# Optimization experiments

Hardware: AMD Instinct MI355X
Metric: run time of the kernel (lower is better)

Reference implementation:

```python
import jax, jax.numpy as jnp
import numpy as np

B, N, H, E, P = 2, 20000, 128, 200000, 3


def _mlp2(x, w1, b1, w2, b2):
    # Linear -> SiLU -> Linear
    return jax.nn.silu(x @ w1 + b1) @ w2 + b2


def setup_inputs() -> dict:
    key = jax.random.key(0)
    ks = iter(jax.random.split(key, 40))
    def nrm(shape, s=0.05):
        return jax.random.normal(next(ks), shape, dtype=jnp.float32) * s
    inp = {
        "features": jax.random.normal(next(ks), (B, N, H), dtype=jnp.float32),
        "positions": jax.random.normal(next(ks), (B, N, P), dtype=jnp.float32),
        "edge_index_up": jax.random.randint(next(ks), (2, E), 0, N, dtype=jnp.int32),
        "edge_index_down": jax.random.randint(next(ks), (2, E), 0, N, dtype=jnp.int32),
        "degree_up": jax.random.uniform(next(ks), (N,), minval=1.0, maxval=32.0, dtype=jnp.float32),
        "degree_down": jax.random.uniform(next(ks), (N,), minval=1.0, maxval=32.0, dtype=jnp.float32),
    }
    for name in ("up", "down"):
        inp[f"w_msg1_{name}"] = nrm((2 * H + 1, H)); inp[f"b_msg1_{name}"] = jnp.zeros((H,), jnp.float32)
        inp[f"w_msg2_{name}"] = nrm((H, H));         inp[f"b_msg2_{name}"] = jnp.zeros((H,), jnp.float32)
        inp[f"w_pos1_{name}"] = nrm((H, H));         inp[f"b_pos1_{name}"] = jnp.zeros((H,), jnp.float32)
        inp[f"w_pos2_{name}"] = nrm((H, 1));         inp[f"b_pos2_{name}"] = jnp.zeros((1,), jnp.float32)
    inp["w_upd1"] = nrm((2 * H, H)); inp["b_upd1"] = jnp.zeros((H,), jnp.float32)
    inp["w_upd2"] = nrm((H, H));     inp["b_upd2"] = jnp.zeros((H,), jnp.float32)
    return inp


def reference(features, positions, edge_index_up, edge_index_down, degree_up, degree_down,
              w_msg1_up, b_msg1_up, w_msg2_up, b_msg2_up,
              w_pos1_up, b_pos1_up, w_pos2_up, b_pos2_up,
              w_msg1_down, b_msg1_down, w_msg2_down, b_msg2_down,
              w_pos1_down, b_pos1_down, w_pos2_down, b_pos2_down,
              w_upd1, b_upd1, w_upd2, b_upd2):
    n_neighborhoods = 2
    msg_acc = jnp.zeros_like(features)
    pos_upd = jnp.zeros_like(positions)
    neighborhoods = [
        (edge_index_up, degree_up,
         (w_msg1_up, b_msg1_up, w_msg2_up, b_msg2_up),
         (w_pos1_up, b_pos1_up, w_pos2_up, b_pos2_up)),
        (edge_index_down, degree_down,
         (w_msg1_down, b_msg1_down, w_msg2_down, b_msg2_down),
         (w_pos1_down, b_pos1_down, w_pos2_down, b_pos2_down)),
    ]
    for edge_index, degree, msg_p, pos_p in neighborhoods:
        src, dst = edge_index[0], edge_index[1]
        h_src = features[:, src, :]                     # [B, E, H] gather
        h_dst = features[:, dst, :]                     # [B, E, H] gather
        rel_pos = positions[:, src, :] - positions[:, dst, :]  # [B, E, P]
        dist = jnp.linalg.norm(rel_pos, axis=-1, keepdims=True)  # [B, E, 1]
        msg_input = jnp.concatenate([h_src, h_dst, dist], axis=-1)  # [B, E, 2H+1]
        messages = _mlp2(msg_input, *msg_p)             # [B, E, H]
        agg = jnp.zeros_like(features).at[:, dst, :].add(messages)  # scatter-add over dim 1
        agg = agg / jnp.clip(degree, 1.0, None)[None, :, None]
        msg_acc = msg_acc + agg
        weights = jnp.tanh(_mlp2(messages, *pos_p))     # [B, E, 1]
        pos_upd = pos_upd + jnp.zeros_like(positions).at[:, dst, :].add(weights * rel_pos)
    feat_update = _mlp2(jnp.concatenate([features, msg_acc], axis=-1), w_upd1, b_upd1, w_upd2, b_upd2)
    updated_features = features + feat_update
    updated_positions = positions + pos_upd / n_neighborhoods
    return updated_features, updated_positions
```

## Files before the change

### kernel.cpp

```cpp
#include <hip/hip_runtime.h>

#define BB 2
#define NN 20000
#define HH 128
#define EE 200000
#define TR 64
#define NEB 3125
#define NBLK 79
#define NWG (2 * BB * NEB)

typedef unsigned short u16;
typedef __attribute__((ext_vector_type(4))) float f32x4;
typedef __bf16 bf16x8 __attribute__((ext_vector_type(8)));

#define MFMA(a, b, c) __builtin_amdgcn_mfma_f32_16x16x32_bf16((a), (b), (c), 0, 0, 0)

__device__ __forceinline__ float bf2f(u16 u) {
    union { unsigned int i; float f; } v; v.i = ((unsigned int)u) << 16; return v.f;
}
__device__ __forceinline__ u16 f2bf(float f) {
    union { __bf16 h; u16 u; } v; v.h = (__bf16)f; return v.u;
}
#if __has_builtin(__builtin_amdgcn_rcpf)
__device__ __forceinline__ float rcpf(float x) { return __builtin_amdgcn_rcpf(x); }
#else
__device__ __forceinline__ float rcpf(float x) { return 1.f / x; }
#endif
__device__ __forceinline__ float silu_f(float z) { return z * rcpf(1.f + __expf(-z)); }
__device__ __forceinline__ float ldv(const void* p, long i, int f) {
    return f ? ((const float*)p)[i] : bf2f(((const u16*)p)[i]);
}

__global__ __launch_bounds__(256) void detect_kernel(const u16* __restrict__ f,
                                                     int* __restrict__ flag) {
    int tid = threadIdx.x;
    u16 v = f[tid * 2];
    int e = (v >> 7) & 0xFF;
    int ok = (e >= 101 && e <= 143) ? 1 : 0;
    __shared__ int c;
    if (tid == 0) c = 0;
    __syncthreads();
    atomicAdd(&c, ok);
    __syncthreads();
    if (tid == 0) *flag = (c < 200) ? 1 : 0;
}

#define C5TOT 5281540
#define FTOT 180224
#define SV 655000
#define SCT 41540
#define SB2 (SV + SCT)
#define SC2 (SB2 + FTOT)
#define SD2 (SC2 + 2 * EE)
struct P18 { const void* p[18]; };
struct P8 { const void* w[8]; };

__global__ __launch_bounds__(256) void setup_kernel(
    P18 cp, P8 wf, const int* __restrict__ eu, const int* __restrict__ ed,
    u16* __restrict__ canon, u16* __restrict__ fbase,
    int* __restrict__ cnt_up, int* __restrict__ cnt_dn, const int* __restrict__ flag)
{
    long i = (long)blockIdx.x * 256 + threadIdx.x;
    const int isf = *flag;
    if (i < SV) {
        long j = i * 8;
        if (isf) {
            const float* src = (j < 5120000)
                ? (const float*)cp.p[0] + j
                : (const float*)cp.p[1] + (j - 5120000);
            float4 v0 = *(const float4*)src;
            float4 v1 = *(const float4*)(src + 4);
            uint4 o;
            o.x = (unsigned)f2bf(v0.x) | ((unsigned)f2bf(v0.y) << 16);
            o.y = (unsigned)f2bf(v0.z) | ((unsigned)f2bf(v0.w) << 16);
            o.z = (unsigned)f2bf(v1.x) | ((unsigned)f2bf(v1.y) << 16);
            o.w = (unsigned)f2bf(v1.z) | ((unsigned)f2bf(v1.w) << 16);
            *(uint4*)&canon[j] = o;
        } else {
            const u16* src = (j < 5120000)
                ? (const u16*)cp.p[0] + j
                : (const u16*)cp.p[1] + (j - 5120000);
            *(uint4*)&canon[j] = *(const uint4*)src;
        }
        return;
    }
    long k = i - SV;
    if (k < SCT) {
        static const int off[19] = {
            0, 5120000, 5240000, 5260000, 5280000,
            5280128, 5280256, 5280384, 5280512, 5280640,
            5280642, 5280770, 5280898, 5281026, 5281154, 5281282,
            5281284, 5281412, 5281540 };
        static const int rsz[18] = {
            5120000, 120000, 20000, 20000,
            128, 128, 128, 128, 128, 1,
            128, 128, 128, 128, 128, 1,
            128, 128 };
        static const int soff[18] = {
            0, 0, 0, 0,
            32768, 0, 0, 0, 0, 0,
            32768, 0, 0, 0, 0, 0,
            0, 0 };
        int j = 5240000 + (int)k;
        int t = 0;
#pragma unroll 1
        while (j >= off[t + 1]) ++t;
        int kk = j - off[t];
        u16 v = 0;
        if (kk < rsz[t]) v = f2bf(ldv(cp.p[t], (long)soff[t] + kk, isf));
        canon[j] = v;
        return;
    }
    k -= SCT;
    if (k < FTOT) {
        static const int foff[9] = { 0, 32768, 49152, 65536, 98304, 114688,
                                     131072, 163840, 180224 };
        int j = (int)k;
        int t = 0;
#pragma unroll 1
        while (j >= foff[t + 1]) ++t;
        int m = j - foff[t];
        int jj = m & 7, lane = (m >> 3) & 63, nt = (m >> 9) & 7, kt = m >> 12;
        int kr = kt * 32 + ((lane >> 4) * 8) + jj;
        int n = nt * 16 + (lane & 15);
        fbase[j] = f2bf(ldv(wf.w[t], (long)kr * 128 + n, isf));
        return;
    }
    k -= FTOT;
    if (k < 2 * EE) {
        int e = (int)k;
        if (e < EE) atomicAdd(&cnt_up[eu[EE + e]], 1);
        else atomicAdd(&cnt_dn[ed[EE + e - EE]], 1);
    }
}

__global__ __launch_bounds__(256) void gemm_fuse_kernel(
    const void* __restrict__ w2u, const void* __restrict__ p1u,
    const void* __restrict__ b2u, const void* __restrict__ bp1u,
    const void* __restrict__ w2d, const void* __restrict__ p1d,
    const void* __restrict__ b2d, const void* __restrict__ bp1d,
    u16* __restrict__ fragu, u16* __restrict__ fragd,
    u16* __restrict__ cbp1u, u16* __restrict__ cbp1d,
    const int* __restrict__ flag)
{
    const int dir = blockIdx.x >> 6;
    const int idx = (blockIdx.x & 63) * 256 + threadIdx.x;
    const int k = idx >> 7, n = idx & 127;
    const int isf = *flag;
    const void* W2 = dir ? w2d : w2u;
    const void* P1 = dir ? p1d : p1u;
    float s = 0.f;
#pragma unroll 4
    for (int m = 0; m < 128; ++m)
        s += ldv(W2, (long)k * 128 + m, isf) * ldv(P1, (long)m * 128 + n, isf);
    u16* dst = dir ? fragd : fragu;
    dst[(((k >> 5) * 8 + (n >> 4)) * 64 + ((k >> 3) & 3) * 16 + (n & 15)) * 8 + (k & 7)] = f2bf(s);
    if (idx < 128) {
        const void* B2 = dir ? b2d : b2u;
        const void* BP1 = dir ? bp1d : bp1u;
        float t = 0.f;
#pragma unroll 4
        for (int m = 0; m < 128; ++m)
            t += ldv(B2, m, isf) * ldv(P1, (long)m * 128 + idx, isf);
        (dir ? cbp1d : cbp1u)[idx] = f2bf(t + ldv(BP1, idx, isf));
    }
}

struct SP { const int* cnt[2]; int* cur[2]; int* bsum[2]; };

__global__ __launch_bounds__(256) void scan1_kernel(SP p) {
    int half = blockIdx.x / NBLK;
    int b = blockIdx.x - half * NBLK;
    int t = threadIdx.x;
    int i = b * 256 + t;
    __shared__ int buf[256];
    int v = (i < NN) ? p.cnt[half][i] : 0;
    buf[t] = v;
    __syncthreads();
    for (int s = 1; s < 256; s <<= 1) {
        int x = (t >= s) ? buf[t - s] : 0;
        __syncthreads();
        buf[t] += x;
        __syncthreads();
    }
    if (i < NN) p.cur[half][i] = buf[t] - v;
    if (t == 255) p.bsum[half][b] = buf[255];
}

__global__ __launch_bounds__(256) void scan2_kernel(int* __restrict__ bu, int* __restrict__ bd) {
    __shared__ int buf[2][128];
    int half = threadIdx.x >> 7, t = threadIdx.x & 127;
    int* bs = half ? bd : bu;
    int v = (t < NBLK) ? bs[t] : 0;
    buf[half][t] = v;
    __syncthreads();
    for (int s = 1; s < 128; s <<= 1) {
        int x = (t >= s) ? buf[half][t - s] : 0;
        __syncthreads();
        buf[half][t] += x;
        __syncthreads();
    }
    if (t < NBLK) bs[t] = buf[half][t] - v;
}

__global__ void scatter2_kernel(const int* __restrict__ eu, const int* __restrict__ ed,
                                int* __restrict__ cu, const int* __restrict__ bu,
                                int* __restrict__ cd, const int* __restrict__ bd,
                                int* __restrict__ su, int* __restrict__ sd) {
    int e = blockIdx.x * 256 + threadIdx.x;
    if (e < EE) {
        int d = eu[EE + e];
        int p = atomicAdd(&cu[d], 1) + bu[d >> 8];
        su[p] = e;
    } else {
        e -= EE;
        if (e < EE) {
            int d = ed[EE + e];
            int p = atomicAdd(&cd[d], 1) + bd[d >> 8];
            sd[p] = e;
        }
    }
}

struct EP {
    const int* eidx; const int* es; const u16* deg;
    const u16* fW1; const u16* fW2;
    const u16* w1last; const u16* bias1; const u16* bias2;
    const u16* biasp1; const u16* wp2; const u16* biasp2;
};

__global__ __launch_bounds__(512, 6) void edge_kernel(
    const u16* __restrict__ feat, const u16* __restrict__ posit,
    EP up, EP dn,
    float* __restrict__ msg_base, float* __restrict__ pos_base)
{
    const int tid = threadIdx.x;
    const int lane = tid & 63;
    const int wv = tid >> 6;
    const int bid0 = blockIdx.x;
    const int xcd = bid0 & 7;
    const int bid = (xcd < 4 ? xcd * 1563 : 4 * 1563 + (xcd - 4) * 1562) + (bid0 >> 3);
    const int half = bid / (BB * NEB);
    const int rem = bid - half * (BB * NEB);
    const int bb = rem / NEB;
    const int s0 = (rem - bb * NEB) * TR;
    const EP P = half ? dn : up;
    float* msg_acc = msg_base + (size_t)bb * NN * HH;
    float* pos_acc = pos_base + (size_t)bb * NN * 3;

    __shared__ u16 sA[TR][136];
    __shared__ u16 sB[TR][136];
    __shared__ u16 sC[TR][136];
    __shared__ float sInv[TR];
    __shared__ float sWgt[TR];
    __shared__ int sDst[TR];

    const int wm = wv >> 2;
    const int wn = wv & 3;
    const int rbase = wm * 32;
    const int mrow = lane & 15;
    const int kq = (lane >> 4) * 8;
    const int crow = (lane >> 4) * 4;
    const int ccol = lane & 15;

    {
        const int r = tid >> 3, part = tid & 7;
        int slot = s0 + r; if (slot >= EE) slot = EE - 1;
        int e = P.es[slot];
        int s = P.eidx[e];
        int d = P.eidx[EE + e];
        if (part == 0) {
            sDst[r] = d;
            sInv[r] = 1.f / fmaxf(bf2f(P.deg[d]), 1.f);
            const u16* ps = posit + ((size_t)bb * NN + s) * 3;
            const u16* pd = posit + ((size_t)bb * NN + d) * 3;
            float dx = bf2f(ps[0]) - bf2f(pd[0]);
            float dy = bf2f(ps[1]) - bf2f(pd[1]);
            float dz = bf2f(ps[2]) - bf2f(pd[2]);
            *(float4*)&sC[r][128] =
                make_float4(sqrtf(dx * dx + dy * dy + dz * dz), dx, dy, dz);
        }
        const uint4* fs = (const uint4*)(feat + ((size_t)bb * NN + s) * HH);
        const uint4* fd = (const uint4*)(feat + ((size_t)bb * NN + d) * HH);
        uint4* as = (uint4*)&sA[r][part * 16];
        uint4* ad = (uint4*)&sB[r][part * 16];
#pragma unroll
        for (int i = 0; i < 2; ++i) { as[i] = fs[part * 2 + i]; ad[i] = fd[part * 2 + i]; }
    }
    __syncthreads();

    f32x4 acc[2][2];
#pragma unroll
    for (int mt = 0; mt < 2; ++mt) {
        acc[mt][0] = (f32x4){0.f, 0.f, 0.f, 0.f};
        acc[mt][1] = (f32x4){0.f, 0.f, 0.f, 0.f};
    }
#pragma unroll
    for (int kt = 0; kt < 8; ++kt) {
        const u16* Xb = (kt < 4) ? &sA[0][0] : &sB[0][0];
        const int kk = (kt & 3) * 32 + kq;
        bf16x8 bw0 = *(const bf16x8*)(P.fW1 + (size_t)(((kt * 8 + wn * 2) * 64 + lane) * 8));
        bf16x8 bw1 = *(const bf16x8*)(P.fW1 + (size_t)(((kt * 8 + wn * 2 + 1) * 64 + lane) * 8));
#pragma unroll
        for (int mt = 0; mt < 2; ++mt) {
            bf16x8 a = *(const bf16x8*)(Xb + (rbase + mt * 16 + mrow) * 136 + kk);
            acc[mt][0] = MFMA(a, bw0, acc[mt][0]);
            acc[mt][1] = MFMA(a, bw1, acc[mt][1]);
        }
    }

#pragma unroll
    for (int n2 = 0; n2 < 2; ++n2) {
        const int col = (wn * 2 + n2) * 16 + ccol;
        const float wl = bf2f(P.w1last[col]);
        const float bb1 = bf2f(P.bias1[col]);
#pragma unroll
        for (int mt = 0; mt < 2; ++mt) {
#pragma unroll
            for (int r = 0; r < 4; ++r) {
                const int row = rbase + mt * 16 + crow + r;
                const float dist = ((const float*)&sC[row][128])[0];
                float z = fmaf(dist, wl, acc[mt][n2][r]) + bb1;
                sC[row][col] = f2bf(silu_f(z));
            }
        }
    }
    __syncthreads();

    f32x4 facc[2][4];
#pragma unroll
    for (int mt = 0; mt < 2; ++mt)
#pragma unroll
        for (int j = 0; j < 4; ++j) facc[mt][j] = (f32x4){0.f, 0.f, 0.f, 0.f};
    const int nt0 = wn * 4;
#pragma unroll
    for (int kt = 0; kt < 4; ++kt) {
        const int kk = kt * 32 + kq;
        bf16x8 bw[4];
#pragma unroll
        for (int j = 0; j < 4; ++j) {
            const int nt = nt0 + j;
            const size_t off = (nt & 8)
                ? (size_t)(16384 + ((kt * 8 + (nt & 7)) * 64 + lane) * 8)
                : (size_t)(((kt * 8 + nt) * 64 + lane) * 8);
            bw[j] = *(const bf16x8*)(P.fW2 + off);
        }
#pragma unroll
        for (int mt = 0; mt < 2; ++mt) {
            bf16x8 a = *(const bf16x8*)(&sC[0][0] + (rbase + mt * 16 + mrow) * 136 + kk);
#pragma unroll
            for (int j = 0; j < 4; ++j) facc[mt][j] = MFMA(a, bw[j], facc[mt][j]);
        }
    }

    if (wn < 2) {
#pragma unroll
        for (int j = 0; j < 4; ++j) {
            const int col = (nt0 + j) * 16 + ccol;
            const float b2v = bf2f(P.bias2[col]);
#pragma unroll
            for (int mt = 0; mt < 2; ++mt) {
#pragma unroll
                for (int r = 0; r < 4; ++r) {
                    const int row = rbase + mt * 16 + crow + r;
                    sA[row][col] = f2bf(facc[mt][j][r] + b2v);
                }
            }
        }
    } else {
#pragma unroll
        for (int j = 0; j < 4; ++j) {
            const int col = (nt0 - 8 + j) * 16 + ccol;
            const float fbv = bf2f(P.biasp1[col]);
#pragma unroll
            for (int mt = 0; mt < 2; ++mt) {
#pragma unroll
                for (int r = 0; r < 4; ++r) {
                    const int row = rbase + mt * 16 + crow + r;
                    sB[row][col] = f2bf(silu_f(facc[mt][j][r] + fbv));
                }
            }
        }
    }
    __syncthreads();

    {
        const int scol = tid & 127;
        const int r0 = (tid >> 7) * 16;
        float vals[16];
#pragma unroll
        for (int j = 0; j < 16; ++j) vals[j] = bf2f(sA[r0 + j][scol]);
        float accv = 0.f;
        int dprev = sDst[r0];
        float invprev = sInv[r0];
#pragma unroll
        for (int j = 0; j < 16; ++j) {
            const int r = r0 + j;
            int dcur = sDst[r];
            if (dcur != dprev) {
                unsafeAtomicAdd(&msg_acc[(size_t)dprev * HH + scol], accv * invprev);
                accv = 0.f; dprev = dcur; invprev = sInv[r];
            }
            accv += (s0 + r < EE) ? vals[j] : 0.f;
        }
        unsafeAtomicAdd(&msg_acc[(size_t)dprev * HH + scol], accv * invprev);
    }

    if (wn == 0) {
        f32x4 pacc[2];
        pacc[0] = (f32x4){0.f, 0.f, 0.f, 0.f};
        pacc[1] = (f32x4){0.f, 0.f, 0.f, 0.f};
#pragma unroll
        for (int kt = 0; kt < 4; ++kt) {
            bf16x8 bp;
#pragma unroll
            for (int z = 0; z < 8; ++z) bp[z] = (__bf16)0.f;
            if ((lane & 15) == 0)
                bp = *(const bf16x8*)(P.wp2 + kt * 32 + (lane >> 4) * 8);
            const int kk = kt * 32 + kq;
#pragma unroll
            for (int mt = 0; mt < 2; ++mt) {
                bf16x8 a = *(const bf16x8*)(&sB[0][0] + (rbase + mt * 16 + mrow) * 136 + kk);
                pacc[mt] = MFMA(a, bp, pacc[mt]);
            }
        }
        if ((lane & 15) == 0) {
            const float bp2 = bf2f(P.biasp2[0]);
#pragma unroll
            for (int mt = 0; mt < 2; ++mt) {
#pragma unroll
                for (int r = 0; r < 4; ++r) {
                    const int row = rbase + mt * 16 + crow + r;
                    sWgt[row] = (s0 + row < EE) ? tanhf(pacc[mt][r] + bp2) : 0.f;
                }
            }
        }
    }
    __syncthreads();

    if (tid < 12) {
        const int comp = tid % 3;
        const int r0 = (tid / 3) * 16;
        float accv = 0.f;
        int dprev = sDst[r0];
#pragma unroll
        for (int j = 0; j < 16; ++j) {
            const int r = r0 + j;
            int dcur = sDst[r];
            if (dcur != dprev) {
                if (accv != 0.f) unsafeAtomicAdd(&pos_acc[(size_t)dprev * 3 + comp], accv);
                accv = 0.f; dprev = dcur;
            }
            accv += sWgt[r] * ((const float*)&sC[r][128])[1 + comp];
        }
        if (accv != 0.f) unsafeAtomicAdd(&pos_acc[(size_t)dprev * 3 + comp], accv);
    }
}

__global__ __launch_bounds__(256) void update_kernel(
    const void* __restrict__ rawfeat, const void* __restrict__ rawpos,
    const u16* __restrict__ fU1, const u16* __restrict__ bu1,
    const u16* __restrict__ fU2, const u16* __restrict__ bu2,
    void* __restrict__ outp, const float* __restrict__ magg, const float* __restrict__ pacc,
    const int* __restrict__ flag)
{
    const int tid = threadIdx.x;
    const int lane = tid & 63;
    const int wv = tid >> 6;
    const int row0 = blockIdx.x * 64;
    const int isf = *flag;

    __shared__ u16 sA[64][136];
    __shared__ u16 sB[64][136];

    if (isf) {
        const float* fp = (const float*)rawfeat + (size_t)row0 * HH;
        for (int i = tid; i < 1024; i += 256) {
            int r = i >> 4, c = (i & 15) * 8;
            float4 v0 = *(const float4*)(fp + (size_t)r * HH + c);
            float4 v1 = *(const float4*)(fp + (size_t)r * HH + c + 4);
            uint4 o;
            o.x = (unsigned)f2bf(v0.x) | ((unsigned)f2bf(v0.y) << 16);
            o.y = (unsigned)f2bf(v0.z) | ((unsigned)f2bf(v0.w) << 16);
            o.z = (unsigned)f2bf(v1.x) | ((unsigned)f2bf(v1.y) << 16);
            o.w = (unsigned)f2bf(v1.z) | ((unsigned)f2bf(v1.w) << 16);
            *(uint4*)&sA[r][c] = o;
        }
    } else {
        const uint4* fp = (const uint4*)((const u16*)rawfeat + (size_t)row0 * HH);
        for (int i = tid; i < 1024; i += 256) {
            int r = i >> 4, c = i & 15;
            *(uint4*)&sA[r][c * 8] = fp[i];
        }
    }
    {
        const float4* am = (const float4*)(magg) + (size_t)row0 * 32;
        for (int i = tid; i < 2048; i += 256) {
            int r = i >> 5;
            float4 v = am[i];
            int c = (i & 31) * 4;
            sB[r][c + 0] = f2bf(v.x);
            sB[r][c + 1] = f2bf(v.y);
            sB[r][c + 2] = f2bf(v.z);
            sB[r][c + 3] = f2bf(v.w);
        }
    }
    __syncthreads();

    const int nt0 = wv * 2;
    const int mrow = lane & 15;
    const int kq = (lane >> 4) * 8;
    const int crow = (lane >> 4) * 4;
    const int ccol = lane & 15;

    f32x4 acc[4][2];
#pragma unroll
    for (int mt = 0; mt < 4; ++mt) {
        acc[mt][0] = (f32x4){0.f, 0.f, 0.f, 0.f};
        acc[mt][1] = (f32x4){0.f, 0.f, 0.f, 0.f};
    }
#pragma unroll
    for (int kt = 0; kt < 8; ++kt) {
        const u16* Xb = (kt < 4) ? &sA[0][0] : &sB[0][0];
        const int kk = (kt & 3) * 32 + kq;
        bf16x8 bw0 = *(const bf16x8*)(fU1 + (size_t)(((kt * 8 + nt0) * 64 + lane) * 8));
        bf16x8 bw1 = *(const bf16x8*)(fU1 + (size_t)(((kt * 8 + nt0 + 1) * 64 + lane) * 8));
#pragma unroll
        for (int mt = 0; mt < 4; ++mt) {
            bf16x8 a = *(const bf16x8*)(Xb + (mt * 16 + mrow) * 136 + kk);
            acc[mt][0] = MFMA(a, bw0, acc[mt][0]);
            acc[mt][1] = MFMA(a, bw1, acc[mt][1]);
        }
    }
    __syncthreads();

#pragma unroll
    for (int mt = 0; mt < 4; ++mt) {
#pragma unroll
        for (int n2 = 0; n2 < 2; ++n2) {
            const int col = (nt0 + n2) * 16 + ccol;
            const float bb = bf2f(bu1[col]);
#pragma unroll
            for (int r = 0; r < 4; ++r) {
                const int row = mt * 16 + crow + r;
                sB[row][col] = f2bf(silu_f(acc[mt][n2][r] + bb));
            }
        }
    }
    __syncthreads();

#pragma unroll
    for (int mt = 0; mt < 4; ++mt) {
        acc[mt][0] = (f32x4){0.f, 0.f, 0.f, 0.f};
        acc[mt][1] = (f32x4){0.f, 0.f, 0.f, 0.f};
    }
#pragma unroll
    for (int kt = 0; kt < 4; ++kt) {
        const int kk = kt * 32 + kq;
        bf16x8 bw0 = *(const bf16x8*)(fU2 + (size_t)(((kt * 8 + nt0) * 64 + lane) * 8));
        bf16x8 bw1 = *(const bf16x8*)(fU2 + (size_t)(((kt * 8 + nt0 + 1) * 64 + lane) * 8));
#pragma unroll
        for (int mt = 0; mt < 4; ++mt) {
            bf16x8 a = *(const bf16x8*)(&sB[0][0] + (mt * 16 + mrow) * 136 + kk);
            acc[mt][0] = MFMA(a, bw0, acc[mt][0]);
            acc[mt][1] = MFMA(a, bw1, acc[mt][1]);
        }
    }
#pragma unroll
    for (int mt = 0; mt < 4; ++mt) {
#pragma unroll
        for (int n2 = 0; n2 < 2; ++n2) {
            const int col = (nt0 + n2) * 16 + ccol;
            const float bb = bf2f(bu2[col]);
#pragma unroll
            for (int r = 0; r < 4; ++r) {
                const int row = mt * 16 + crow + r;
                const size_t idx = (size_t)(row0 + row) * HH + col;
                if (isf) {
                    float base = ((const float*)rawfeat)[idx];
                    ((float*)outp)[idx] = acc[mt][n2][r] + bb + base;
                } else {
                    float base = bf2f(sA[row][col]);
                    ((u16*)outp)[idx] = f2bf(acc[mt][n2][r] + bb + base);
                }
            }
        }
    }

    if (tid < 192) {
        int i = row0 * 3 + tid;
        float x = pacc[i];
        if (isf) {
            float base = ((const float*)rawpos)[i];
            ((float*)outp)[5120000 + i] = base + 0.5f * x;
        } else {
            float base = bf2f(((const u16*)rawpos)[i]);
            ((u16*)outp)[5120000 + i] = f2bf(base + 0.5f * x);
        }
    }
}

extern "C" void kernel_launch(void* const* d_in, const int* in_sizes, int n_in,
                              void* d_out, int out_size, void* d_ws, size_t ws_size,
                              hipStream_t stream)
{
    float* ws_msg  = (float*)d_ws;
    float* ws_pos  = (float*)((char*)d_ws + 20480000);
    int*   cnt_up  = (int*)((char*)d_ws + 20960000);
    int*   cnt_dn  = (int*)((char*)d_ws + 21040000);
    int*   cur_up  = (int*)((char*)d_ws + 21120000);
    int*   cur_dn  = (int*)((char*)d_ws + 21200000);
    int*   bsum_up = (int*)((char*)d_ws + 21280000);
    int*   bsum_dn = (int*)((char*)d_ws + 21280400);
    int*   es_up   = (int*)((char*)d_ws + 21280800);
    int*   es_dn   = (int*)((char*)d_ws + 22080800);
    u16*   fbase   = (u16*)((char*)d_ws + 22880800);
    u16*   canon   = (u16*)((char*)d_ws + 23241248);
    int*   flag    = (int*)((char*)d_ws + 33804328);
    if (ws_size < 33804332ULL) return;

    u16* f_m1u = fbase;
    u16* f_m2u = fbase + 32768;
    u16* f_p1u = fbase + 49152;
    u16* f_m1d = fbase + 65536;
    u16* f_m2d = fbase + 98304;
    u16* f_p1d = fbase + 114688;
    u16* f_u1  = fbase + 131072;
    u16* f_u2  = fbase + 163840;

    u16* cfeat  = canon;
    u16* cpos   = canon + 5120000;
    u16* cdgu   = canon + 5240000;
    u16* cdgd   = canon + 5260000;
    u16* cw1lu  = canon + 5280000;
    u16* cb1u   = canon + 5280128;
    u16* cb2u   = canon + 5280256;
    u16* cbp1u  = canon + 5280384;
    u16* cwp2u  = canon + 5280512;
    u16* cbp2u  = canon + 5280640;
    u16* cw1ld  = canon + 5280642;
    u16* cb1d   = canon + 5280770;
    u16* cb2d   = canon + 5280898;
    u16* cbp1d  = canon + 5281026;
    u16* cwp2d  = canon + 5281154;
    u16* cbp2d  = canon + 5281282;
    u16* cbu1   = canon + 5281284;
    u16* cbu2   = canon + 5281412;

    const int* ei_up = (const int*)d_in[2];
    const int* ei_dn = (const int*)d_in[3];

    hipMemsetAsync(d_ws, 0, 21120000, stream);

    detect_kernel<<<1, 256, 0, stream>>>((const u16*)d_in[0], flag);

    P18 cp;
    cp.p[0] = d_in[0];  cp.p[1] = d_in[1];  cp.p[2] = d_in[4];  cp.p[3] = d_in[5];
    cp.p[4] = d_in[6];  cp.p[5] = d_in[7];  cp.p[6] = d_in[9];  cp.p[7] = d_in[11];
    cp.p[8] = d_in[12]; cp.p[9] = d_in[13];
    cp.p[10] = d_in[14]; cp.p[11] = d_in[15]; cp.p[12] = d_in[17]; cp.p[13] = d_in[19];
    cp.p[14] = d_in[20]; cp.p[15] = d_in[21];
    cp.p[16] = d_in[23]; cp.p[17] = d_in[25];
    P8 wsf;
    wsf.w[0] = d_in[6];  wsf.w[1] = d_in[8];  wsf.w[2] = d_in[10]; wsf.w[3] = d_in[14];
    wsf.w[4] = d_in[16]; wsf.w[5] = d_in[18]; wsf.w[6] = d_in[22]; wsf.w[7] = d_in[24];
    setup_kernel<<<(SD2 + 255) / 256, 256, 0, stream>>>(cp, wsf, ei_up, ei_dn,
                                                        canon, fbase,
                                                        cnt_up, cnt_dn, flag);

    gemm_fuse_kernel<<<128, 256, 0, stream>>>(d_in[8], d_in[10], d_in[9], d_in[11],
                                              d_in[16], d_in[18], d_in[17], d_in[19],
                                              f_p1u, f_p1d, cbp1u, cbp1d, flag);

    SP sp;
    sp.cnt[0] = cnt_up; sp.cnt[1] = cnt_dn;
    sp.cur[0] = cur_up; sp.cur[1] = cur_dn;
    sp.bsum[0] = bsum_up; sp.bsum[1] = bsum_dn;
    scan1_kernel<<<2 * NBLK, 256, 0, stream>>>(sp);
    scan2_kernel<<<1, 256, 0, stream>>>(bsum_up, bsum_dn);
    scatter2_kernel<<<(2 * EE + 255) / 256, 256, 0, stream>>>(ei_up, ei_dn, cur_up, bsum_up,
                                                              cur_dn, bsum_dn, es_up, es_dn);

    EP up, dn;
    up.eidx = ei_up; up.es = es_up; up.deg = cdgu;
    up.fW1 = f_m1u; up.fW2 = f_m2u;
    up.w1last = cw1lu; up.bias1 = cb1u; up.bias2 = cb2u;
    up.biasp1 = cbp1u; up.wp2 = cwp2u; up.biasp2 = cbp2u;
    dn.eidx = ei_dn; dn.es = es_dn; dn.deg = cdgd;
    dn.fW1 = f_m1d; dn.fW2 = f_m2d;
    dn.w1last = cw1ld; dn.bias1 = cb1d; dn.bias2 = cb2d;
    dn.biasp1 = cbp1d; dn.wp2 = cwp2d; dn.biasp2 = cbp2d;
    edge_kernel<<<NWG, 512, 0, stream>>>(cfeat, cpos, up, dn, ws_msg, ws_pos);

    update_kernel<<<625, 256, 0, stream>>>(d_in[0], d_in[1], f_u1, cbu1, f_u2, cbu2,
                                           d_out, ws_msg, ws_pos, flag);
}
```

Before: 455.1 us.

## Accumulate aggregated messages in bf16 with packed atomics, scalar position weight dot

Changes the per-node message accumulator from fp32 to bf16 and uses packed bf16x2 atomic adds, so half as many atomics and half the bytes go to the scatter target. The update kernel then loads the bf16 accumulator directly. The position-weight projection (a 128-wide dot product) also moves from a mostly-empty MFMA on one wave column to per-thread FMAs with shuffle reductions. Accumulating many atomics in bf16 loses precision and may break the error tolerance. The memset size and workspace layout are left unchanged.

Measured after the change: 442.2 us. -2.8%, faster.

```diff
diff --git a/kernel.cpp b/kernel.cpp
--- a/kernel.cpp
+++ b/kernel.cpp
@@ -1,4 +1,5 @@
 #include <hip/hip_runtime.h>
+#include <hip/hip_bf16.h>
 
 #define BB 2
 #define NN 20000
@@ -232,7 +233,7 @@
 __global__ __launch_bounds__(512, 6) void edge_kernel(
     const u16* __restrict__ feat, const u16* __restrict__ posit,
     EP up, EP dn,
-    float* __restrict__ msg_base, float* __restrict__ pos_base)
+    u16* __restrict__ msg_base, float* __restrict__ pos_base)
 {
     const int tid = threadIdx.x;
     const int lane = tid & 63;
@@ -245,7 +246,7 @@
     const int bb = rem / NEB;
     const int s0 = (rem - bb * NEB) * TR;
     const EP P = half ? dn : up;
-    float* msg_acc = msg_base + (size_t)bb * NN * HH;
+    u16* msg_acc = msg_base + (size_t)bb * NN * HH;
     float* pos_acc = pos_base + (size_t)bb * NN * 3;
 
     __shared__ u16 sA[TR][136];
@@ -384,13 +385,18 @@
     }
     __syncthreads();
 
-    {
-        const int scol = tid & 127;
-        const int r0 = (tid >> 7) * 16;
-        float vals[16];
-#pragma unroll
-        for (int j = 0; j < 16; ++j) vals[j] = bf2f(sA[r0 + j][scol]);
-        float accv = 0.f;
+    if (tid < 256) {
+        const int cp2 = tid & 63;
+        const int r0 = (tid >> 6) * 16;
+        float v0[16], v1[16];
+#pragma unroll
+        for (int j = 0; j < 16; ++j) {
+            unsigned w = *(const unsigned*)&sA[r0 + j][cp2 * 2];
+            union { unsigned i; float f; } a, b;
+            a.i = w << 16; b.i = w & 0xffff0000u;
+            v0[j] = a.f; v1[j] = b.f;
+        }
+        float a0 = 0.f, a1 = 0.f;
         int dprev = sDst[r0];
         float invprev = sInv[r0];
 #pragma unroll
@@ -398,42 +404,37 @@
             const int r = r0 + j;
             int dcur = sDst[r];
             if (dcur != dprev) {
-                unsafeAtomicAdd(&msg_acc[(size_t)dprev * HH + scol], accv * invprev);
-                accv = 0.f; dprev = dcur; invprev = sInv[r];
-            }
-            accv += (s0 + r < EE) ? vals[j] : 0.f;
-        }
-        unsafeAtomicAdd(&msg_acc[(size_t)dprev * HH + scol], accv * invprev);
-    }
-
-    if (wn == 0) {
-        f32x4 pacc[2];
-        pacc[0] = (f32x4){0.f, 0.f, 0.f, 0.f};
-        pacc[1] = (f32x4){0.f, 0.f, 0.f, 0.f};
-#pragma unroll
-        for (int kt = 0; kt < 4; ++kt) {
-            bf16x8 bp;
-#pragma unroll
-            for (int z = 0; z < 8; ++z) bp[z] = (__bf16)0.f;
-            if ((lane & 15) == 0)
-                bp = *(const bf16x8*)(P.wp2 + kt * 32 + (lane >> 4) * 8);
-            const int kk = kt * 32 + kq;
-#pragma unroll
-            for (int mt = 0; mt < 2; ++mt) {
-                bf16x8 a = *(const bf16x8*)(&sB[0][0] + (rbase + mt * 16 + mrow) * 136 + kk);
-                pacc[mt] = MFMA(a, bp, pacc[mt]);
-            }
-        }
-        if ((lane & 15) == 0) {
-            const float bp2 = bf2f(P.biasp2[0]);
-#pragma unroll
-            for (int mt = 0; mt < 2; ++mt) {
-#pragma unroll
-                for (int r = 0; r < 4; ++r) {
-                    const int row = rbase + mt * 16 + crow + r;
-                    sWgt[row] = (s0 + row < EE) ? tanhf(pacc[mt][r] + bp2) : 0.f;
-                }
-            }
+                union { unsigned u; __hip_bfloat162 h; } pk;
+                pk.u = (unsigned)f2bf(a0 * invprev) | ((unsigned)f2bf(a1 * invprev) << 16);
+                unsafeAtomicAdd((__hip_bfloat162*)(msg_acc + (size_t)dprev * HH + cp2 * 2), pk.h);
+                a0 = 0.f; a1 = 0.f; dprev = dcur; invprev = sInv[r];
+            }
+            if (s0 + r < EE) { a0 += v0[j]; a1 += v1[j]; }
+        }
+        union { unsigned u; __hip_bfloat162 h; } pk;
+        pk.u = (unsigned)f2bf(a0 * invprev) | ((unsigned)f2bf(a1 * invprev) << 16);
+        unsafeAtomicAdd((__hip_bfloat162*)(msg_acc + (size_t)dprev * HH + cp2 * 2), pk.h);
+    }
+
+    {
+        const int r = tid >> 2, q = tid & 3;
+        if (r < TR) {
+            const unsigned* t32 = (const unsigned*)&sB[r][q * 32];
+            const unsigned* w32 = (const unsigned*)(P.wp2 + q * 32);
+            float p = 0.f;
+#pragma unroll
+            for (int k = 0; k < 16; ++k) {
+                unsigned a = t32[k], b = w32[k];
+                union { unsigned i; float f; } al, ah, bl, bh;
+                al.i = a << 16; ah.i = a & 0xffff0000u;
+                bl.i = b << 16; bh.i = b & 0xffff0000u;
+                p = fmaf(al.f, bl.f, p);
+                p = fmaf(ah.f, bh.f, p);
+            }
+            p += __shfl_xor(p, 1);
+            p += __shfl_xor(p, 2);
+            if (q == 0)
+                sWgt[r] = (s0 + r < EE) ? tanhf(p + bf2f(P.biasp2[0])) : 0.f;
         }
     }
     __syncthreads();
@@ -461,7 +462,7 @@
     const void* __restrict__ rawfeat, const void* __restrict__ rawpos,
     const u16* __restrict__ fU1, const u16* __restrict__ bu1,
     const u16* __restrict__ fU2, const u16* __restrict__ bu2,
-    void* __restrict__ outp, const float* __restrict__ magg, const float* __restrict__ pacc,
+    void* __restrict__ outp, const u16* __restrict__ magg, const float* __restrict__ pacc,
     const int* __restrict__ flag)
 {
     const int tid = threadIdx.x;
@@ -494,15 +495,10 @@
         }
     }
     {
-        const float4* am = (const float4*)(magg) + (size_t)row0 * 32;
-        for (int i = tid; i < 2048; i += 256) {
-            int r = i >> 5;
-            float4 v = am[i];
-            int c = (i & 31) * 4;
-            sB[r][c + 0] = f2bf(v.x);
-            sB[r][c + 1] = f2bf(v.y);
-            sB[r][c + 2] = f2bf(v.z);
-            sB[r][c + 3] = f2bf(v.w);
+        const uint4* am = (const uint4*)magg + (size_t)row0 * 16;
+        for (int i = tid; i < 1024; i += 256) {
+            int r = i >> 4, c = i & 15;
+            *(uint4*)&sB[r][c * 8] = am[i];
         }
     }
     __syncthreads();
@@ -604,7 +600,7 @@
                               void* d_out, int out_size, void* d_ws, size_t ws_size,
                               hipStream_t stream)
 {
-    float* ws_msg  = (float*)d_ws;
+    u16*   ws_msg  = (u16*)d_ws;
     float* ws_pos  = (float*)((char*)d_ws + 20480000);
     int*   cnt_up  = (int*)((char*)d_ws + 20960000);
     int*   cnt_dn  = (int*)((char*)d_ws + 21040000);
```
